# Performance work log

Measured on AMD Instinct MI355X. Metric: run time of the kernel, lower is better.

Reference implementation:

```python
import jax, jax.numpy as jnp
import numpy as np

NEG_SLOPE = 0.2  # HANConv default negative_slope
N_NODES = 100000
N_REL = 8
N_EDGES = 200000
N_LABEL = 131072
C_IN = 128
H1 = 128
H2 = 128


def _segment_softmax(logits, seg, num_segments):
    # PyG softmax(src, index): exp(src - max_per_seg) / (sum_per_seg + 1e-16)
    m = jax.ops.segment_max(logits, seg, num_segments=num_segments)
    m = jnp.where(jnp.isfinite(m), m, 0.0)  # empty segments -> 0
    e = jnp.exp(logits - m[seg])
    s = jax.ops.segment_sum(e, seg, num_segments=num_segments)
    return e / (s[seg] + 1e-16)


def _han_layer(x, edge_index, proj_w, proj_b, att_src, att_dst, q, klin_w, klin_b):
    # x: [N, Cin]; edge_index: [R, 2, E]; att_src/att_dst: [R, D]; klin_w: [D, D] (torch [out,in])
    N = x.shape[0]
    h = x @ proj_w + proj_b            # [N, D] shared projection for node type 'node'
    a_src = h @ att_src.T              # [N, R] per-node src attention logits
    a_dst = h @ att_dst.T              # [N, R]

    def per_rel(eidx, a_s, a_d):
        src, dst = eidx[0], eidx[1]
        alpha = jax.nn.leaky_relu(a_s[src] + a_d[dst], NEG_SLOPE)     # [E]
        alpha = _segment_softmax(alpha, dst, N)                        # softmax over in-neighbors
        out = jax.ops.segment_sum(alpha[:, None] * h[src], dst, num_segments=N)  # [N, D]
        return jax.nn.relu(out)        # HANConv applies relu per edge-type output

    outs = jax.vmap(per_rel, in_axes=(0, 1, 1))(edge_index, a_src, a_dst)  # [R, N, D]
    # semantic attention across edge types (group())
    score = jnp.einsum('d,rd->r', q, jnp.tanh(outs @ klin_w.T + klin_b).mean(axis=1))
    attn = jax.nn.softmax(score)       # [R]
    return jnp.einsum('r,rnd->nd', attn, outs)


def setup_inputs() -> dict:
    key = jax.random.key(0)
    ks = jax.random.split(key, 24)
    f32 = jnp.float32

    def lin_w(k, fin, fout):
        return (jax.random.normal(k, (fin, fout), f32) / np.sqrt(fin)).astype(f32)

    inp = {
        'x': jax.random.normal(ks[0], (N_NODES, C_IN), f32),
        'edge_index': jax.random.randint(ks[1], (N_REL, 2, N_EDGES), 0, N_NODES, jnp.int32),
        'edge_label_index': jax.random.randint(ks[2], (2, N_LABEL), 0, N_NODES, jnp.int32),
        # HANConv layer 1 params
        'w1': lin_w(ks[3], C_IN, H1), 'b1': jnp.zeros((H1,), f32),
        'asrc1': jax.random.normal(ks[4], (N_REL, H1), f32) / np.sqrt(H1),
        'adst1': jax.random.normal(ks[5], (N_REL, H1), f32) / np.sqrt(H1),
        'q1': jax.random.normal(ks[6], (H1,), f32) / np.sqrt(H1),
        'kw1': lin_w(ks[7], H1, H1).T, 'kb1': jnp.zeros((H1,), f32),
        # HANConv layer 2 params
        'w2': lin_w(ks[8], H1, H2), 'b2': jnp.zeros((H2,), f32),
        'asrc2': jax.random.normal(ks[9], (N_REL, H2), f32) / np.sqrt(H2),
        'adst2': jax.random.normal(ks[10], (N_REL, H2), f32) / np.sqrt(H2),
        'q2': jax.random.normal(ks[11], (H2,), f32) / np.sqrt(H2),
        'kw2': lin_w(ks[12], H2, H2).T, 'kb2': jnp.zeros((H2,), f32),
        # link-score head
        'post_w': lin_w(ks[13], H2, 2), 'post_b': jnp.zeros((2,), f32),
    }
    return inp


def reference(x, edge_index, edge_label_index,
              w1, b1, asrc1, adst1, q1, kw1, kb1,
              w2, b2, asrc2, adst2, q2, kw2, kb2,
              post_w, post_b):
    h = jax.nn.relu(_han_layer(x, edge_index, w1, b1, asrc1, adst1, q1, kw1, kb1))
    h = jax.nn.relu(_han_layer(h, edge_index, w2, b2, asrc2, adst2, q2, kw2, kb2))
    h_had = h[edge_label_index[0]] * h[edge_label_index[1]]   # [L, H2]
    logits = h_had @ post_w + post_b                          # [L, 2]
    return logits.sum(axis=-1)                                # [L]
```

## Files before the change

kernel.cpp:

```cpp
#include <hip/hip_runtime.h>

#define NN 100000
#define NR 8
#define NE 200000
#define NL 131072
#define NSEG (NR*NN)
#define NB_SCAN 782
#define NPAD (NB_SCAN*1024)

typedef __attribute__((ext_vector_type(8))) short short8;
typedef __attribute__((ext_vector_type(4))) float floatx4;

__device__ __forceinline__ unsigned short f2bf(float f) {
    unsigned u = __float_as_uint(f);
    unsigned r = (u + 0x7fff + ((u >> 16) & 1)) >> 16;
    return (unsigned short)r;
}
__device__ __forceinline__ float bf2f(unsigned short s) {
    return __uint_as_float(((unsigned)s) << 16);
}

__device__ __forceinline__ unsigned enc8(float x) {
    unsigned u = __float_as_uint(x);
    unsigned s = (u >> 24) & 0x80;
    unsigned a = u & 0x7fffffff;
    unsigned r = a + 0x7FFFF + ((a >> 20) & 1);
    int em = (int)(r >> 20) - 928;
    em = em < 8 ? 8 : em;
    em = em > 127 ? 127 : em;
    return s | (unsigned)em;
}
__device__ __forceinline__ float dec8(unsigned b) {
    unsigned t = b & 0x7f;
    unsigned mag = (t << 20) + 0x3A000000u;
    unsigned sg = (b & 0x80) << 24;
    return __uint_as_float(mag | sg);
}

__global__ void transpose128(const float* __restrict__ in, float* __restrict__ out) {
    int idx = blockIdx.x * 256 + threadIdx.x;
    int j = idx >> 7, k = idx & 127;
    out[idx] = in[k * 128 + j];
}

__global__ void cast_bf16(const float* __restrict__ src, unsigned short* __restrict__ dst) {
    size_t idx = ((size_t)blockIdx.x * 256 + threadIdx.x) * 4;
    float4 v = *(const float4*)(src + idx);
    ushort4 o;
    o.x = f2bf(v.x); o.y = f2bf(v.y); o.z = f2bf(v.z); o.w = f2bf(v.w);
    *(ushort4*)(dst + idx) = o;
}

__global__ void hist_kernel(const int* __restrict__ ei, int* __restrict__ counts) {
    int idx = blockIdx.x * 256 + threadIdx.x;
    if (idx >= NR * NE) return;
    int r = idx / NE, e = idx - r * NE;
    int dst = ei[(size_t)r * 2 * NE + NE + e];
    atomicAdd(&counts[r * NN + dst], 1);
}

__global__ __launch_bounds__(256) void scan_k1(const int* __restrict__ counts,
                                               int* __restrict__ rowptr,
                                               int* __restrict__ bsums) {
    __shared__ int wsum[4];
    int t = threadIdx.x, lane = t & 63, w = t >> 6;
    int base = blockIdx.x * 1024 + t * 4;
    int c0 = counts[base], c1 = counts[base + 1], c2 = counts[base + 2], c3 = counts[base + 3];
    int s = c0 + c1 + c2 + c3;
    int inc = s;
#pragma unroll
    for (int off = 1; off < 64; off <<= 1) { int v = __shfl_up(inc, off); if (lane >= off) inc += v; }
    if (lane == 63) wsum[w] = inc;
    __syncthreads();
    int wbase = 0;
    for (int k = 0; k < w; ++k) wbase += wsum[k];
    int ex = wbase + inc - s;
    rowptr[base]     = ex;
    rowptr[base + 1] = ex + c0;
    rowptr[base + 2] = ex + c0 + c1;
    rowptr[base + 3] = ex + c0 + c1 + c2;
    if (t == 255) bsums[blockIdx.x] = wbase + inc;
}

__global__ __launch_bounds__(256) void scan_k2(int* __restrict__ bsums, int nb) {
    __shared__ int wsum[4];
    __shared__ int carry_s;
    int t = threadIdx.x, lane = t & 63, w = t >> 6;
    if (t == 0) carry_s = 0;
    __syncthreads();
    for (int base = 0; base < nb; base += 256) {
        int i = base + t;
        int v = (i < nb) ? bsums[i] : 0;
        int inc = v;
#pragma unroll
        for (int off = 1; off < 64; off <<= 1) { int u = __shfl_up(inc, off); if (lane >= off) inc += u; }
        if (lane == 63) wsum[w] = inc;
        __syncthreads();
        int wbase = carry_s;
        for (int k = 0; k < w; ++k) wbase += wsum[k];
        if (i < nb) bsums[i] = wbase + inc - v;
        __syncthreads();
        if (t == 0) carry_s += wsum[0] + wsum[1] + wsum[2] + wsum[3];
        __syncthreads();
    }
}

__global__ void scan_k3(int* __restrict__ rowptr, const int* __restrict__ bsums) {
    int i = blockIdx.x * 256 + threadIdx.x;
    if (i <= NSEG) rowptr[i] += bsums[i >> 10];
}

__global__ void fill_kernel(const int* __restrict__ ei, const int* __restrict__ rowptr,
                            int* __restrict__ cursor, int* __restrict__ es_raw) {
    int idx = blockIdx.x * 256 + threadIdx.x;
    if (idx >= NR * NE) return;
    int r = idx / NE, e = idx - r * NE;
    int src = ei[(size_t)r * 2 * NE + e];
    int dst = ei[(size_t)r * 2 * NE + NE + e];
    int g = r * NN + dst;
    int pos = rowptr[g] + atomicAdd(&cursor[g], 1);
    es_raw[2 * pos] = src;
}

__global__ __launch_bounds__(256, 3) void gemm_proj(
    const float* __restrict__ A, const float* __restrict__ B,
    const float* __restrict__ bias, float* __restrict__ out, int nrows)
{
    __shared__ float As[128][36];
    __shared__ float Bs[128][36];
    const int tid = threadIdx.x;
    const int row0 = blockIdx.x * 128;
    const int cg = tid & 15;
    const int nb = (tid >> 4) * 8;

    float acc[8][8];
#pragma unroll
    for (int i = 0; i < 8; ++i)
#pragma unroll
        for (int j = 0; j < 8; ++j) acc[i][j] = 0.f;

    for (int k0 = 0; k0 < 128; k0 += 32) {
#pragma unroll
        for (int i = 0; i < 4; ++i) {
            int fi = tid + i * 256;
            int rw = fi >> 3, kq = fi & 7;
            int n = row0 + rw;
            float4 v = make_float4(0.f, 0.f, 0.f, 0.f);
            if (n < nrows) v = *(const float4*)(A + (size_t)n * 128 + k0 + kq * 4);
            *(float4*)&As[rw][kq * 4] = v;
            float4 w = *(const float4*)(B + rw * 128 + k0 + kq * 4);
            *(float4*)&Bs[rw][kq * 4] = w;
        }
        __syncthreads();
#pragma unroll 2
        for (int kq = 0; kq < 8; ++kq) {
            float4 wv[8];
#pragma unroll
            for (int j = 0; j < 8; ++j) wv[j] = *(const float4*)&Bs[cg + 16 * j][kq * 4];
#pragma unroll
            for (int i = 0; i < 8; ++i) {
                float4 xv = *(const float4*)&As[nb + i][kq * 4];
#pragma unroll
                for (int j = 0; j < 8; ++j)
                    acc[i][j] += xv.x * wv[j].x + xv.y * wv[j].y
                               + xv.z * wv[j].z + xv.w * wv[j].w;
            }
        }
        __syncthreads();
    }
#pragma unroll
    for (int i = 0; i < 8; ++i) {
        int n = row0 + nb + i;
        if (n < nrows) {
#pragma unroll
            for (int j = 0; j < 8; ++j) {
                int d = cg + 16 * j;
                out[(size_t)n * 128 + d] = acc[i][j] + bias[d];
            }
        }
    }
}

__global__ __launch_bounds__(512) void fused_score3(
    const int* __restrict__ rowptr, const int2* __restrict__ es,
    const unsigned char* __restrict__ h8,
    const unsigned short* __restrict__ kw16, const float* __restrict__ kb,
    const float* __restrict__ q, float* __restrict__ score)
{
    __shared__ unsigned short Os[64][136];
    __shared__ float redbuf[8];
    const int t = threadIdx.x;
    const int r = blockIdx.y;
    const int row0 = blockIdx.x * 64;
    const int l = t & 7, nl = t >> 3;

    float acc[16];
#pragma unroll
    for (int i = 0; i < 16; ++i) acc[i] = 0.f;

    int n = row0 + nl;
    if (n < NN) {
        int g = r * NN + n;
        int p0 = rowptr[g], p1 = rowptr[g + 1];
        int2 ep[4];
#pragma unroll
        for (int i = 0; i < 4; ++i) {
            int idx = min(p0 + i, p1 - 1); idx = max(idx, 0);
            ep[i] = es[idx];
            if (p0 + i >= p1) ep[i].y = 0;
        }
        uint4 hv[4];
#pragma unroll
        for (int i = 0; i < 4; ++i)
            hv[i] = *(const uint4*)(h8 + (size_t)ep[i].x * 128 + l * 16);
#pragma unroll
        for (int i = 0; i < 4; ++i) {
            float al = __int_as_float(ep[i].y);
            const unsigned* up = (const unsigned*)&hv[i];
#pragma unroll
            for (int w = 0; w < 4; ++w) {
                unsigned u = up[w];
                acc[w * 4 + 0] += al * dec8(u & 0xff);
                acc[w * 4 + 1] += al * dec8((u >> 8) & 0xff);
                acc[w * 4 + 2] += al * dec8((u >> 16) & 0xff);
                acc[w * 4 + 3] += al * dec8(u >> 24);
            }
        }
        for (int e = p0 + 4; e < p1; ++e) {
            int2 ep2 = es[e];
            float al = __int_as_float(ep2.y);
            uint4 hq = *(const uint4*)(h8 + (size_t)ep2.x * 128 + l * 16);
            const unsigned* up = (const unsigned*)&hq;
#pragma unroll
            for (int w = 0; w < 4; ++w) {
                unsigned u = up[w];
                acc[w * 4 + 0] += al * dec8(u & 0xff);
                acc[w * 4 + 1] += al * dec8((u >> 8) & 0xff);
                acc[w * 4 + 2] += al * dec8((u >> 16) & 0xff);
                acc[w * 4 + 3] += al * dec8(u >> 24);
            }
        }
    }
    unsigned short ov[16];
#pragma unroll
    for (int i = 0; i < 16; ++i) ov[i] = f2bf(fmaxf(acc[i], 0.f));
    *(short8*)&Os[nl][l * 16]     = *(short8*)&ov[0];
    *(short8*)&Os[nl][l * 16 + 8] = *(short8*)&ov[8];
    __syncthreads();

    const int wave = t >> 6, lane = t & 63;
    const int W = wave >> 1, dth = wave & 1;
    const int quad = lane >> 4, l16 = lane & 15;
    short8 a[4];
#pragma unroll
    for (int kc = 0; kc < 4; ++kc)
        a[kc] = *(const short8*)&Os[W * 16 + l16][quad * 8 + kc * 32];

    float s = 0.f;
#pragma unroll
    for (int dti = 0; dti < 4; ++dti) {
        int dt = dth * 4 + dti;
        const unsigned short* brow = kw16 + (size_t)(dt * 16 + l16) * 128 + quad * 8;
        floatx4 accv = {0.f, 0.f, 0.f, 0.f};
#pragma unroll
        for (int kc = 0; kc < 4; ++kc) {
            short8 b = *(const short8*)(brow + kc * 32);
            accv = __builtin_amdgcn_mfma_f32_16x16x32_bf16(a[kc], b, accv, 0, 0, 0);
        }
        int d = dt * 16 + l16;
        float kbv = kb[d], qv = q[d];
#pragma unroll
        for (int reg = 0; reg < 4; ++reg) {
            int node = row0 + W * 16 + quad * 4 + reg;
            if (node < NN) {
                float y = accv[reg] + kbv;
                float e2 = __expf(2.f * y);
                float tn = 1.f - 2.f * __builtin_amdgcn_rcpf(e2 + 1.f);
                s += tn * qv;
            }
        }
    }
    for (int off = 32; off > 0; off >>= 1) s += __shfl_down(s, off);
    if (lane == 0) redbuf[wave] = s;
    __syncthreads();
    if (t == 0) {
        float tot = 0.f;
#pragma unroll
        for (int i = 0; i < 8; ++i) tot += redbuf[i];
        atomicAdd(score + r, tot);
    }
}

__global__ __launch_bounds__(256) void att_kernel(
    const float* __restrict__ h, const float* __restrict__ asrc_w,
    const float* __restrict__ adst_w, float* __restrict__ a_src,
    float* __restrict__ a_dst, unsigned char* __restrict__ h8)
{
    __shared__ float hs[16][128];
    int n0 = blockIdx.x * 16;
#pragma unroll
    for (int i = 0; i < 2; ++i) {
        int fi = threadIdx.x + i * 256;
        int n = fi >> 5, kq = fi & 31;
        float4 v = make_float4(0.f, 0.f, 0.f, 0.f);
        if (n0 + n < NN) v = *(const float4*)(h + (size_t)(n0 + n) * 128 + kq * 4);
        *(float4*)&hs[n][kq * 4] = v;
    }
    __syncthreads();
    int n = threadIdx.x >> 4, rr = threadIdx.x & 15;
    int r = rr & 7; int isd = rr >> 3;
    const float* w = (isd ? adst_w : asrc_w) + r * 128;
    float acc = 0.f;
#pragma unroll
    for (int kq = 0; kq < 32; ++kq) {
        float4 hv = *(const float4*)&hs[n][kq * 4];
        float4 wv = ((const float4*)w)[kq];
        acc += hv.x * wv.x + hv.y * wv.y + hv.z * wv.z + hv.w * wv.w;
    }
    if (n0 + n < NN) (isd ? a_dst : a_src)[r * NN + n0 + n] = acc;

    int dq = rr * 8;
    if (n0 + n < NN) {
        unsigned lo = 0, hi = 0;
#pragma unroll
        for (int k = 0; k < 4; ++k) lo |= enc8(hs[n][dq + k]) << (8 * k);
#pragma unroll
        for (int k = 0; k < 4; ++k) hi |= enc8(hs[n][dq + 4 + k]) << (8 * k);
        *(uint2*)(h8 + (size_t)(n0 + n) * 128 + dq) = make_uint2(lo, hi);
    }
}

__global__ void softmax_csr(const int* __restrict__ rowptr, int2* __restrict__ es,
                            const float* __restrict__ a_src, const float* __restrict__ a_dst,
                            float* __restrict__ score)
{
    int g = blockIdx.x * 256 + threadIdx.x;
    if (g < NR) score[g] = 0.f;
    if (g >= NSEG) return;
    int p0 = rowptr[g], p1 = rowptr[g + 1];
    if (p0 == p1) return;
    int r = g / NN;
    float ad = a_dst[g];
    const float* as = a_src + (size_t)r * NN;
    float m = -1e30f;
    for (int i = p0; i < p1; ++i) {
        float l = as[es[i].x] + ad;
        l = l > 0.f ? l : 0.2f * l;
        es[i].y = __float_as_int(l);
        m = fmaxf(m, l);
    }
    float s = 0.f;
    for (int i = p0; i < p1; ++i) {
        float e = __expf(__int_as_float(es[i].y) - m);
        es[i].y = __float_as_int(e);
        s += e;
    }
    float inv = __builtin_amdgcn_rcpf(s + 1e-16f);
    for (int i = p0; i < p1; ++i)
        es[i].y = __float_as_int(__int_as_float(es[i].y) * inv);
}

__global__ __launch_bounds__(256, 3) void combine_csr(
    const int* __restrict__ rowptr, const int2* __restrict__ es,
    const float* __restrict__ h, const float* __restrict__ score,
    float* __restrict__ comb)
{
    __shared__ float attn[NR];
    __shared__ float lds[4][64][17];
    int t = threadIdx.x;
    if (t == 0) {
        float sc[NR]; float m = -1e30f;
        for (int r = 0; r < NR; ++r) { sc[r] = score[r] * (1.0f / NN); m = fmaxf(m, sc[r]); }
        float den = 0.f;
        for (int r = 0; r < NR; ++r) { sc[r] = __expf(sc[r] - m); den += sc[r]; }
        for (int r = 0; r < NR; ++r) attn[r] = sc[r] / den;
    }
    __syncthreads();

    int nl = t >> 6;
    int n = blockIdx.x * 4 + nl;
    int L = t & 63;
    int r = L >> 3;
    int d0 = (L & 7) * 16;
    float a[16];
#pragma unroll
    for (int i = 0; i < 16; ++i) a[i] = 0.f;
    {
        int g = r * NN + n;
        int p0 = rowptr[g], p1 = rowptr[g + 1];
        int2 ep[4];
#pragma unroll
        for (int i = 0; i < 4; ++i) {
            int idx = min(p0 + i, p1 - 1); idx = max(idx, 0);
            ep[i] = es[idx];
            if (p0 + i >= p1) ep[i].y = 0;
        }
        float4 hv[4][4];
#pragma unroll
        for (int i = 0; i < 4; ++i) {
            const float* hp = h + (size_t)ep[i].x * 128 + d0;
            hv[i][0] = *(const float4*)hp;
            hv[i][1] = *(const float4*)(hp + 4);
            hv[i][2] = *(const float4*)(hp + 8);
            hv[i][3] = *(const float4*)(hp + 12);
        }
#pragma unroll
        for (int i = 0; i < 4; ++i) {
            float al = __int_as_float(ep[i].y);
#pragma unroll
            for (int j = 0; j < 4; ++j) {
                a[4*j]   += al * hv[i][j].x; a[4*j+1] += al * hv[i][j].y;
                a[4*j+2] += al * hv[i][j].z; a[4*j+3] += al * hv[i][j].w;
            }
        }
        for (int e = p0 + 4; e < p1; ++e) {
            int2 ep2 = es[e];
            float al = __int_as_float(ep2.y);
            const float* hp = h + (size_t)ep2.x * 128 + d0;
            float4 v0 = *(const float4*)hp;
            float4 v1 = *(const float4*)(hp + 4);
            float4 v2 = *(const float4*)(hp + 8);
            float4 v3 = *(const float4*)(hp + 12);
            a[0]+=al*v0.x; a[1]+=al*v0.y; a[2]+=al*v0.z;  a[3]+=al*v0.w;
            a[4]+=al*v1.x; a[5]+=al*v1.y; a[6]+=al*v1.z;  a[7]+=al*v1.w;
            a[8]+=al*v2.x; a[9]+=al*v2.y; a[10]+=al*v2.z; a[11]+=al*v2.w;
            a[12]+=al*v3.x;a[13]+=al*v3.y;a[14]+=al*v3.z; a[15]+=al*v3.w;
        }
    }
    float w = attn[r];
    float* dst = &lds[nl][L][0];
#pragma unroll
    for (int i = 0; i < 16; ++i) dst[i] = w * fmaxf(a[i], 0.f);
    __syncthreads();

    int o = L >> 3, j = L & 7;
    float s0 = 0.f, s1 = 0.f;
#pragma unroll
    for (int rr = 0; rr < NR; ++rr) {
        s0 += lds[nl][rr * 8 + o][2 * j];
        s1 += lds[nl][rr * 8 + o][2 * j + 1];
    }
    *(float2*)(comb + (size_t)n * 128 + 2 * L) = make_float2(s0, s1);
}

__global__ __launch_bounds__(256) void head_kernel(
    const float* __restrict__ hfin, const int* __restrict__ eli,
    const float* __restrict__ pw, const float* __restrict__ pb,
    float* __restrict__ out)
{
    int t = threadIdx.x;
    int l = blockIdx.x * 4 + (t >> 6);
    int d0 = (t & 63) * 2;
    int a = eli[l], b = eli[NL + l];
    float2 ha = *(const float2*)(hfin + (size_t)a * 128 + d0);
    float2 hb = *(const float2*)(hfin + (size_t)b * 128 + d0);
    float w0 = pw[d0 * 2] + pw[d0 * 2 + 1];
    float w1 = pw[d0 * 2 + 2] + pw[d0 * 2 + 3];
    float v = ha.x * hb.x * w0 + ha.y * hb.y * w1;
    for (int off = 32; off > 0; off >>= 1) v += __shfl_down(v, off);
    if ((t & 63) == 0) out[l] = v + pb[0] + pb[1];
}

extern "C" void kernel_launch(void* const* d_in, const int* in_sizes, int n_in,
                              void* d_out, int out_size, void* d_ws, size_t ws_size,
                              hipStream_t stream)
{
    const float* x     = (const float*)d_in[0];
    const int*   ei    = (const int*)d_in[1];
    const int*   eli   = (const int*)d_in[2];
    const float* w1    = (const float*)d_in[3];
    const float* b1    = (const float*)d_in[4];
    const float* asrc1 = (const float*)d_in[5];
    const float* adst1 = (const float*)d_in[6];
    const float* q1    = (const float*)d_in[7];
    const float* kw1   = (const float*)d_in[8];
    const float* kb1   = (const float*)d_in[9];
    const float* w2    = (const float*)d_in[10];
    const float* b2    = (const float*)d_in[11];
    const float* asrc2 = (const float*)d_in[12];
    const float* adst2 = (const float*)d_in[13];
    const float* q2    = (const float*)d_in[14];
    const float* kw2   = (const float*)d_in[15];
    const float* kb2   = (const float*)d_in[16];
    const float* pw    = (const float*)d_in[17];
    const float* pb    = (const float*)d_in[18];
    float* out = (float*)d_out;

    float* ws      = (float*)d_ws;
    float* hA      = ws;
    float* hB      = ws + 12800000ull;
    float* a_src   = ws + 25600000ull;
    float* a_dst   = ws + 26400000ull;
    int2*  es      = (int2*)(ws + 27200000ull);
    int*   rowptr  = (int*)(ws + 30400000ull);
    int*   counts  = (int*)(ws + 31200768ull);
    int*   bsums   = (int*)(ws + 32001536ull);
    float* score   = ws + 32002560ull;
    float* wt      = ws + 32002624ull;
    unsigned short* kw16 = (unsigned short*)(ws + 32019008ull);
    unsigned char* h8 = (unsigned char*)hB;

    hipMemsetAsync(counts, 0, NPAD * sizeof(int), stream);
    hist_kernel<<<6250, 256, 0, stream>>>(ei, counts);
    scan_k1<<<NB_SCAN, 256, 0, stream>>>(counts, rowptr, bsums);
    scan_k2<<<1, 256, 0, stream>>>(bsums, NB_SCAN);
    scan_k3<<<3126, 256, 0, stream>>>(rowptr, bsums);
    hipMemsetAsync(counts, 0, NPAD * sizeof(int), stream);
    fill_kernel<<<6250, 256, 0, stream>>>(ei, rowptr, counts, (int*)es);

    for (int layer = 0; layer < 2; ++layer) {
        const float* Ain  = layer ? hB : x;
        const float* W    = layer ? w2 : w1;
        const float* bb   = layer ? b2 : b1;
        const float* as_w = layer ? asrc2 : asrc1;
        const float* ad_w = layer ? adst2 : adst1;
        const float* qq   = layer ? q2 : q1;
        const float* kw   = layer ? kw2 : kw1;
        const float* kb   = layer ? kb2 : kb1;

        transpose128<<<64, 256, 0, stream>>>(W, wt);
        gemm_proj<<<782, 256, 0, stream>>>(Ain, wt, bb, hA, NN);
        cast_bf16<<<16, 256, 0, stream>>>(kw, kw16);
        att_kernel<<<6250, 256, 0, stream>>>(hA, as_w, ad_w, a_src, a_dst, h8);
        softmax_csr<<<3125, 256, 0, stream>>>(rowptr, es, a_src, a_dst, score);
        fused_score3<<<dim3(1563, NR), 512, 0, stream>>>(rowptr, es, h8,
                                                         kw16, kb, qq, score);
        combine_csr<<<25000, 256, 0, stream>>>(rowptr, es, hA, score, hB);
    }
    head_kernel<<<32768, 256, 0, stream>>>(hB, eli, pw, pb, out);
}
```

Before: 1.430 ms.

## Balance edge aggregation in score kernel with edge-parallel LDS atomics

Replaces the per-node edge loop in the semantic-score kernel with an edge-parallel scheme. Each block's edges are spread evenly across 64 thread slots, each edge finds its destination row by binary search over a shared rowptr slice, and contributions are accumulated into an fp32 LDS tile with atomics. This targets load imbalance from variable in-degree, where one thread octet handled every edge of a node. The cost is many LDS float atomics, an extra zeroing pass and extra barriers.

```diff
diff --git a/kernel.cpp b/kernel.cpp
--- a/kernel.cpp
+++ b/kernel.cpp
@@ -181,80 +181,73 @@
     }
 }
 
-__global__ __launch_bounds__(512) void fused_score3(
+__global__ __launch_bounds__(512) void fused_score4(
     const int* __restrict__ rowptr, const int2* __restrict__ es,
     const unsigned char* __restrict__ h8,
     const unsigned short* __restrict__ kw16, const float* __restrict__ kb,
     const float* __restrict__ q, float* __restrict__ score)
 {
-    __shared__ unsigned short Os[64][136];
+    __shared__ float OsF[64][132];
+    __shared__ int rp[65];
     __shared__ float redbuf[8];
     const int t = threadIdx.x;
     const int r = blockIdx.y;
     const int row0 = blockIdx.x * 64;
-    const int l = t & 7, nl = t >> 3;
-
-    float acc[16];
-#pragma unroll
-    for (int i = 0; i < 16; ++i) acc[i] = 0.f;
-
-    int n = row0 + nl;
-    if (n < NN) {
-        int g = r * NN + n;
-        int p0 = rowptr[g], p1 = rowptr[g + 1];
-        int2 ep[4];
-#pragma unroll
-        for (int i = 0; i < 4; ++i) {
-            int idx = min(p0 + i, p1 - 1); idx = max(idx, 0);
-            ep[i] = es[idx];
-            if (p0 + i >= p1) ep[i].y = 0;
-        }
-        uint4 hv[4];
-#pragma unroll
-        for (int i = 0; i < 4; ++i)
-            hv[i] = *(const uint4*)(h8 + (size_t)ep[i].x * 128 + l * 16);
-#pragma unroll
-        for (int i = 0; i < 4; ++i) {
-            float al = __int_as_float(ep[i].y);
-            const unsigned* up = (const unsigned*)&hv[i];
-#pragma unroll
-            for (int w = 0; w < 4; ++w) {
-                unsigned u = up[w];
-                acc[w * 4 + 0] += al * dec8(u & 0xff);
-                acc[w * 4 + 1] += al * dec8((u >> 8) & 0xff);
-                acc[w * 4 + 2] += al * dec8((u >> 16) & 0xff);
-                acc[w * 4 + 3] += al * dec8(u >> 24);
-            }
-        }
-        for (int e = p0 + 4; e < p1; ++e) {
-            int2 ep2 = es[e];
-            float al = __int_as_float(ep2.y);
-            uint4 hq = *(const uint4*)(h8 + (size_t)ep2.x * 128 + l * 16);
-            const unsigned* up = (const unsigned*)&hq;
-#pragma unroll
-            for (int w = 0; w < 4; ++w) {
-                unsigned u = up[w];
-                acc[w * 4 + 0] += al * dec8(u & 0xff);
-                acc[w * 4 + 1] += al * dec8((u >> 8) & 0xff);
-                acc[w * 4 + 2] += al * dec8((u >> 16) & 0xff);
-                acc[w * 4 + 3] += al * dec8(u >> 24);
-            }
-        }
-    }
-    unsigned short ov[16];
-#pragma unroll
-    for (int i = 0; i < 16; ++i) ov[i] = f2bf(fmaxf(acc[i], 0.f));
-    *(short8*)&Os[nl][l * 16]     = *(short8*)&ov[0];
-    *(short8*)&Os[nl][l * 16 + 8] = *(short8*)&ov[8];
-    __syncthreads();
-
+    const int g0 = r * NN + row0;
+    const int gend = (r + 1) * NN;
+
+    if (t < 65) rp[t] = rowptr[min(g0 + t, gend)];
+    for (int i = t; i < 64 * 132; i += 512) (&OsF[0][0])[i] = 0.f;
+    __syncthreads();
+
+    const int l = t & 7, slot = t >> 3;
+    const int e0 = rp[0], e1 = rp[64];
+    for (int e = e0 + slot; e < e1; e += 64) {
+        int2 ep = es[e];
+        float al = __int_as_float(ep.y);
+        int lo = 0, hi = 64;
+#pragma unroll
+        for (int it = 0; it < 6; ++it) {
+            int mid = (lo + hi) >> 1;
+            if (rp[mid] <= e) lo = mid; else hi = mid;
+        }
+        uint4 hq = *(const uint4*)(h8 + (size_t)ep.x * 128 + l * 16);
+        const unsigned* up = (const unsigned*)&hq;
+        float* orow = &OsF[lo][l * 16];
+#pragma unroll
+        for (int w = 0; w < 4; ++w) {
+            unsigned u = up[w];
+            atomicAdd(orow + w * 4 + 0, al * dec8(u & 0xff));
+            atomicAdd(orow + w * 4 + 1, al * dec8((u >> 8) & 0xff));
+            atomicAdd(orow + w * 4 + 2, al * dec8((u >> 16) & 0xff));
+            atomicAdd(orow + w * 4 + 3, al * dec8(u >> 24));
+        }
+    }
+    __syncthreads();
+
+    {
+        int row = t >> 3;
+        float v[16];
+#pragma unroll
+        for (int i = 0; i < 16; ++i) v[i] = OsF[row][l * 16 + i];
+        __syncthreads();
+        unsigned short* OsU = (unsigned short*)&OsF[0][0];
+        unsigned short ov[16];
+#pragma unroll
+        for (int i = 0; i < 16; ++i) ov[i] = f2bf(fmaxf(v[i], 0.f));
+        *(short8*)&OsU[row * 136 + l * 16]     = *(short8*)&ov[0];
+        *(short8*)&OsU[row * 136 + l * 16 + 8] = *(short8*)&ov[8];
+    }
+    __syncthreads();
+
+    const unsigned short* OsU = (const unsigned short*)&OsF[0][0];
     const int wave = t >> 6, lane = t & 63;
     const int W = wave >> 1, dth = wave & 1;
     const int quad = lane >> 4, l16 = lane & 15;
     short8 a[4];
 #pragma unroll
     for (int kc = 0; kc < 4; ++kc)
-        a[kc] = *(const short8*)&Os[W * 16 + l16][quad * 8 + kc * 32];
+        a[kc] = *(const short8*)&OsU[(W * 16 + l16) * 136 + quad * 8 + kc * 32];
 
     float s = 0.f;
 #pragma unroll
@@ -523,7 +516,7 @@
         cast_bf16<<<16, 256, 0, stream>>>(kw, kw16);
         att_kernel<<<6250, 256, 0, stream>>>(hA, as_w, ad_w, a_src, a_dst, h8);
         softmax_csr<<<3125, 256, 0, stream>>>(rowptr, es, a_src, a_dst, score);
-        fused_score3<<<dim3(1563, NR), 512, 0, stream>>>(rowptr, es, h8,
+        fused_score4<<<dim3(1563, NR), 512, 0, stream>>>(rowptr, es, h8,
                                                          kw16, kb, qq, score);
         combine_csr<<<25000, 256, 0, stream>>>(rowptr, es, hA, score, hB);
     }
```

Measured after the change: 3.132 ms. 119% more time.
